# Optimization experiments

Hardware: AMD Instinct MI355X
Metric: run time of the kernel (lower is better)

Reference implementation:

```python
import jax, jax.numpy as jnp
from jax import lax
import numpy as np

N, L, C, G, K = 8, 4096, 256, 8, 3
GC = C // G
DILATION = 1
OFFSET_SCALE = 1.0
LN_EPS = 1e-6


def setup_inputs() -> dict:
    key = jax.random.key(0)
    ks = jax.random.split(key, 14)
    s = lambda k, shp, sc: jax.random.normal(k, shp, jnp.float32) * sc
    return {
        "x": jax.random.normal(ks[0], (N, L, C), jnp.float32),
        "W_in": s(ks[1], (C, C), (1.0 / C) ** 0.5),      # input_proj (in,out)
        "b_in": jnp.zeros((C,), jnp.float32),
        "conv_w": s(ks[2], (C, 1, K), 0.2),              # depthwise conv (O, I/g, K)
        "conv_b": jnp.zeros((C,), jnp.float32),
        "ln_g": jnp.ones((C,), jnp.float32),
        "ln_b": jnp.zeros((C,), jnp.float32),
        "W_off": s(ks[3], (C, G * K), 0.02),             # offset_linear
        "b_off": s(ks[4], (G * K,), 0.02),
        "W_mask": s(ks[5], (C, G * K), 0.02),            # mask_linear
        "b_mask": s(ks[6], (G * K,), 0.02),
        "W_out": s(ks[7], (C, C), (1.0 / C) ** 0.5),     # output_proj
        "b_out": jnp.zeros((C,), jnp.float32),
    }


def _dcnv3_1d(x, W_in, b_in, conv_w, conv_b, ln_g, ln_b,
              W_off, b_off, W_mask, b_mask, W_out, b_out):
    # x: (N, L, C)
    x_proj = x @ W_in + b_in                                     # (N,L,C)

    # depthwise conv -> LayerNorm(C) -> GELU  (the offset/mask feature branch)
    xc = x.transpose(0, 2, 1)                                    # (N,C,L)
    pad = (K - 1) // 2
    y = lax.conv_general_dilated(
        xc, conv_w, window_strides=(1,), padding=[(pad, pad)],
        dimension_numbers=("NCH", "OIH", "NCH"), feature_group_count=C)
    y = y + conv_b[None, :, None]
    y = y.transpose(0, 2, 1)                                     # (N,L,C)
    mu = y.mean(-1, keepdims=True)
    var = ((y - mu) ** 2).mean(-1, keepdims=True)
    y = (y - mu) * lax.rsqrt(var + LN_EPS) * ln_g + ln_b
    x_feat = jax.nn.gelu(y, approximate=False)                   # torch GELU = exact erf

    offset = (x_feat @ W_off + b_off).reshape(N, L, G, K)
    mask = jax.nn.softmax((x_feat @ W_mask + b_mask).reshape(N, L, G, K), axis=-1)

    # sampling locations (grid_sample with align_corners=True unnormalizes back to loc)
    ref_p = jnp.arange(L, dtype=jnp.float32)                     # (L,)
    lo = float(-((K - 1) // 2))
    hi = float((K - 1) // 2)
    dil_grid = jnp.linspace(lo, hi, K) * DILATION                # (K,)
    loc = ref_p[None, :, None, None] + dil_grid[None, None, None, :] \
          + offset * OFFSET_SCALE                                # (N,L,G,K)
    loc = jnp.remainder(loc, L)                                  # in [0, L)

    # bilinear sample along L with zero padding (matches F.grid_sample, H=1)
    f0 = jnp.floor(loc)
    w1 = loc - f0
    w0 = 1.0 - w1
    i0 = jnp.clip(f0.astype(jnp.int32), 0, L - 1)
    i1 = i0 + 1
    valid1 = (i1 < L)
    i1c = jnp.where(valid1, i1, 0)

    x_g = x_proj.reshape(N, L, G, GC)                            # (N,L,G,gc)
    nidx = jnp.arange(N)[:, None, None, None]
    gidx = jnp.arange(G)[None, None, :, None]
    v0 = x_g[nidx, i0, gidx]                                     # (N,L,G,K,gc)
    v1 = x_g[nidx, i1c, gidx] * valid1[..., None].astype(x_g.dtype)
    sampled = w0[..., None] * v0 + w1[..., None] * v1            # (N,L,G,K,gc)

    out = (sampled * mask[..., None]).sum(axis=3)                # (N,L,G,gc)
    out = out.reshape(N, L, C)
    return out @ W_out + b_out


def reference(x, W_in, b_in, conv_w, conv_b, ln_g, ln_b,
              W_off, b_off, W_mask, b_mask, W_out, b_out):
    return _dcnv3_1d(x, W_in, b_in, conv_w, conv_b, ln_g, ln_b,
                     W_off, b_off, W_mask, b_mask, W_out, b_out)
```

## Files before the change

kernel.cpp:

```cpp
#include <hip/hip_runtime.h>
#include <math.h>

constexpr int LL = 4096;
constexpr int CC = 256;
constexpr int MM = 32768;

typedef unsigned int u32;
typedef unsigned short u16;
typedef __attribute__((ext_vector_type(8))) short bf16x8;
typedef __attribute__((ext_vector_type(4))) float f32x4;

__device__ __forceinline__ u16 f2b(float f) {
    u32 u = __float_as_uint(f);
    u32 r = (u + 0x7fffu + ((u >> 16) & 1u)) >> 16;
    return (u16)r;
}
__device__ __forceinline__ u32 pack2(float a, float b) {
    return (u32)f2b(a) | ((u32)f2b(b) << 16);
}

__device__ __forceinline__ void gl_lds16(const u16* g, u16* l) {
    __builtin_amdgcn_global_load_lds(
        (const __attribute__((address_space(1))) unsigned int*)g,
        (__attribute__((address_space(3))) unsigned int*)l, 16, 0, 0);
}

__global__ __launch_bounds__(256) void conv_prep(
    const float* __restrict__ x, const float* __restrict__ cw,
    const float* __restrict__ cbias, const float* __restrict__ lng,
    const float* __restrict__ lnb, u16* __restrict__ xf,
    const float* __restrict__ W_in, const float* __restrict__ W_out,
    const float* __restrict__ W_off, const float* __restrict__ W_mask,
    u16* __restrict__ Wt_in, u16* __restrict__ Wt_out, u16* __restrict__ Wcomb)
{
    const int bid = blockIdx.x;
    const int t = threadIdx.x;
    if (bid >= 8192) {
        const int b = bid - 8192;
        if (b < 256) {
            Wt_in[b * 256 + t]  = f2b(W_in[t * 256 + b]);
            Wt_out[b * 256 + t] = f2b(W_out[t * 256 + b]);
        } else {
            const int j = b - 256;
            const float v = (j < 24) ? W_off[t * 24 + j] : W_mask[t * 24 + (j - 24)];
            Wcomb[j * 256 + t] = f2b(v);
        }
        return;
    }

    const int i = ((bid & 7) << 10) | (bid >> 3);

    const int wave = t >> 6;
    const int lane = t & 63;
    const int nl = (i << 2) + wave;
    const int l = nl & (LL - 1);
    const int c0 = lane << 2;
    const size_t base = (size_t)nl * CC + c0;

    float4 xc = *(const float4*)&x[base];
    float4 xm = make_float4(0.f, 0.f, 0.f, 0.f);
    float4 xp = make_float4(0.f, 0.f, 0.f, 0.f);
    if (l > 0)      xm = *(const float4*)&x[base - CC];
    if (l < LL - 1) xp = *(const float4*)&x[base + CC];

    float xmv[4] = {xm.x, xm.y, xm.z, xm.w};
    float xcv[4] = {xc.x, xc.y, xc.z, xc.w};
    float xpv[4] = {xp.x, xp.y, xp.z, xp.w};

    float y[4];
    float sum = 0.f, sq = 0.f;
#pragma unroll
    for (int j = 0; j < 4; ++j) {
        const int c = c0 + j;
        float v = fmaf(xmv[j], cw[c * 3 + 0],
                  fmaf(xcv[j], cw[c * 3 + 1],
                  fmaf(xpv[j], cw[c * 3 + 2], cbias[c])));
        y[j] = v;
        sum += v;
        sq  += v * v;
    }
#pragma unroll
    for (int off = 32; off > 0; off >>= 1) {
        sum += __shfl_xor(sum, off);
        sq  += __shfl_xor(sq, off);
    }
    const float mu  = sum * (1.f / CC);
    const float var = sq * (1.f / CC) - mu * mu;
    const float rs  = rsqrtf(var + 1e-6f);

    ushort4 o;
    float ov[4];
#pragma unroll
    for (int j = 0; j < 4; ++j) {
        const int c = c0 + j;
        const float tn = (y[j] - mu) * rs * lng[c] + lnb[c];
        ov[j] = 0.5f * tn * (1.f + erff(tn * 0.70710678118654752f));
    }
    o.x = f2b(ov[0]); o.y = f2b(ov[1]); o.z = f2b(ov[2]); o.w = f2b(ov[3]);
    *(ushort4*)&xf[base] = o;
}

__global__ __launch_bounds__(256, 2) void gemm1(
    const float* __restrict__ x, const u16* __restrict__ Wt_in,
    const float* __restrict__ b_in, u16* __restrict__ xprojb)
{
    __shared__ u16 As[2][128 * 32];
    __shared__ u16 Bs[2][128 * 32];

    const int t = threadIdx.x;
    const int w = t >> 6, lane = t & 63;
    const int lr = lane & 15, lk = lane >> 4;
    const int wm = w >> 1, wn = w & 1;

    const int d = blockIdx.x;
    const int m_t = (d & 7) * 32 + (d >> 4);
    const int n_t = (d >> 3) & 1;
    const int m0 = m_t * 128, n0 = n_t * 128;

    const int srow = lane >> 2;
    const int scol = (lane & 3) * 8;
    const int arow = t >> 1;
    const int akh = (t & 1) * 16;

    f32x4 acc[4][4];
#pragma unroll
    for (int i = 0; i < 4; ++i)
#pragma unroll
        for (int j = 0; j < 4; ++j) acc[i][j] = f32x4{0.f, 0.f, 0.f, 0.f};

    auto STAGE_B = [&](int buf, int kt) {
        const int k0 = kt * 32;
#pragma unroll
        for (int j = 0; j < 2; ++j) {
            const int rr = (w * 2 + j) * 16 + srow;
            gl_lds16(Wt_in + ((size_t)(n0 + rr) << 8) + k0 + scol,
                     &Bs[buf][0] + (w * 2 + j) * 512);
        }
    };
    const float* Abase = x + (size_t)(m0 + arow) * 256 + akh;

    {
        float4 f0 = *(const float4*)(Abase);
        float4 f1 = *(const float4*)(Abase + 4);
        float4 f2 = *(const float4*)(Abase + 8);
        float4 f3 = *(const float4*)(Abase + 12);
        STAGE_B(0, 0);
        u16* dst = &As[0][arow * 32 + akh];
        ((u32*)dst)[0] = pack2(f0.x, f0.y); ((u32*)dst)[1] = pack2(f0.z, f0.w);
        ((u32*)dst)[2] = pack2(f1.x, f1.y); ((u32*)dst)[3] = pack2(f1.z, f1.w);
        ((u32*)dst)[4] = pack2(f2.x, f2.y); ((u32*)dst)[5] = pack2(f2.z, f2.w);
        ((u32*)dst)[6] = pack2(f3.x, f3.y); ((u32*)dst)[7] = pack2(f3.z, f3.w);
    }

#pragma unroll
    for (int kt = 0; kt < 8; ++kt) {
        const int cur = kt & 1;
        __syncthreads();
        float4 f0, f1, f2, f3;
        if (kt < 7) {
            const float* ap = Abase + (kt + 1) * 32;
            f0 = *(const float4*)(ap);
            f1 = *(const float4*)(ap + 4);
            f2 = *(const float4*)(ap + 8);
            f3 = *(const float4*)(ap + 12);
            STAGE_B(cur ^ 1, kt + 1);
        }
        bf16x8 af[4], bfr[4];
#pragma unroll
        for (int mt = 0; mt < 4; ++mt)
            af[mt] = *(const bf16x8*)&As[cur][(wm * 64 + mt * 16 + lr) * 32 + lk * 8];
#pragma unroll
        for (int nt = 0; nt < 4; ++nt)
            bfr[nt] = *(const bf16x8*)&Bs[cur][(wn * 64 + nt * 16 + lr) * 32 + lk * 8];
#pragma unroll
        for (int mt = 0; mt < 4; ++mt)
#pragma unroll
            for (int nt = 0; nt < 4; ++nt)
                acc[mt][nt] = __builtin_amdgcn_mfma_f32_16x16x32_bf16(
                    af[mt], bfr[nt], acc[mt][nt], 0, 0, 0);
        if (kt < 7) {
            u16* dst = &As[cur ^ 1][arow * 32 + akh];
            ((u32*)dst)[0] = pack2(f0.x, f0.y); ((u32*)dst)[1] = pack2(f0.z, f0.w);
            ((u32*)dst)[2] = pack2(f1.x, f1.y); ((u32*)dst)[3] = pack2(f1.z, f1.w);
            ((u32*)dst)[4] = pack2(f2.x, f2.y); ((u32*)dst)[5] = pack2(f2.z, f2.w);
            ((u32*)dst)[6] = pack2(f3.x, f3.y); ((u32*)dst)[7] = pack2(f3.z, f3.w);
        }
    }

    const int r0 = lk * 4;
#pragma unroll
    for (int nt = 0; nt < 4; ++nt) {
        const int cn = n0 + wn * 64 + nt * 16 + lr;
        const float bv = b_in[cn];
#pragma unroll
        for (int mt = 0; mt < 4; ++mt)
#pragma unroll
            for (int r4 = 0; r4 < 4; ++r4)
                xprojb[(size_t)(m0 + wm * 64 + mt * 16 + r0 + r4) * 256 + cn] =
                    f2b(acc[mt][nt][r4] + bv);
    }
}

__global__ __launch_bounds__(256, 2) void offmask_gemm(
    const u16* __restrict__ xfeatb, const u16* __restrict__ xprojb,
    const u16* __restrict__ Wcomb, const float* __restrict__ boff,
    const float* __restrict__ bmask, const u16* __restrict__ Wt_out,
    const float* __restrict__ b_out, float* __restrict__ out)
{
    __shared__ __align__(16) char s_mem[32768];
    __shared__ uint2 s_pack[512 * 3];
    float* logit = (float*)s_mem;

    const int t = threadIdx.x;
    const int w = t >> 6, lane = t & 63;
    const int lr = lane & 15, lk8 = (lane >> 4) * 8;
    const int r0 = (lane >> 4) * 4;
    const int d = blockIdx.x;
    const int blk = ((d & 7) << 6) | (d >> 3);
    const size_t row0 = (size_t)blk * 64;

    f32x4 pacc[3];
#pragma unroll
    for (int ct = 0; ct < 3; ++ct) pacc[ct] = f32x4{0.f, 0.f, 0.f, 0.f};
    const u16* fbase = xfeatb + (row0 + w * 16 + lr) * 256;
#pragma unroll
    for (int ks = 0; ks < 8; ++ks) {
        const int ke = ks * 32 + lk8;
        bf16x8 a = *(const bf16x8*)(fbase + ke);
#pragma unroll
        for (int ct = 0; ct < 3; ++ct) {
            bf16x8 bfr = *(const bf16x8*)(Wcomb + (size_t)(ct * 16 + lr) * 256 + ke);
            pacc[ct] = __builtin_amdgcn_mfma_f32_16x16x32_bf16(a, bfr, pacc[ct], 0, 0, 0);
        }
    }
#pragma unroll
    for (int ct = 0; ct < 3; ++ct) {
        const int j = ct * 16 + lr;
        const float bj = (j < 24) ? boff[j] : bmask[j - 24];
#pragma unroll
        for (int r4 = 0; r4 < 4; ++r4)
            logit[(w * 16 + r0 + r4) * 50 + j] = pacc[ct][r4] + bj;
    }
    __syncthreads();

#pragma unroll
    for (int pi = 0; pi < 2; ++pi) {
        const int pp = pi * 256 + t;
        const int rw = pp >> 3, g = pp & 7;
        const float* lp = &logit[rw * 50];
        const float m0v = lp[24 + g * 3 + 0];
        const float m1v = lp[24 + g * 3 + 1];
        const float m2v = lp[24 + g * 3 + 2];
        const float mx = fmaxf(m0v, fmaxf(m1v, m2v));
        const float e0 = expf(m0v - mx), e1 = expf(m1v - mx), e2 = expf(m2v - mx);
        const float inv = 1.f / (e0 + e1 + e2);
        const float msk[3] = {e0 * inv, e1 * inv, e2 * inv};
        const float lf = (float)((blk & 63) * 64 + rw);
#pragma unroll
        for (int k = 0; k < 3; ++k) {
            const float loc = lf + (float)(k - 1) + lp[g * 3 + k];
            float r = fmodf(loc, (float)LL);
            if (r < 0.f) r += (float)LL;
            const float f0 = floorf(r);
            int i0 = (int)f0;
            i0 = i0 < 0 ? 0 : (i0 > LL - 1 ? LL - 1 : i0);
            const int i1 = i0 + 1;
            const float w1 = r - f0;
            const bool valid = (i1 < LL);
            union { u32 uw; _Float16 h[2]; } uh;
            uh.h[0] = (_Float16)(msk[k] * (1.f - w1));
            uh.h[1] = (_Float16)(valid ? msk[k] * w1 : 0.f);
            const u32 ij = (u32)i0 | ((u32)(valid ? i1 : 0) << 16);
            s_pack[pp * 3 + k] = make_uint2(uh.uw, ij);
        }
    }
    __syncthreads();

    {
        const int ig = t >> 5, tc = t & 31;
        const int c0 = tc * 8, g4 = tc >> 2;
        const u16* xpn = xprojb + (size_t)(blk >> 6) * LL * 256;
        const int ibeg = ig * 8;
#pragma unroll 4
        for (int i = ibeg; i < ibeg + 8; ++i) {
            const int bidx = (i * 8 + g4) * 3;
            float v[8] = {0.f, 0.f, 0.f, 0.f, 0.f, 0.f, 0.f, 0.f};
#pragma unroll
            for (int k = 0; k < 3; ++k) {
                const uint2 pk = s_pack[bidx + k];
                union { u32 uw; _Float16 h[2]; } uh; uh.uw = pk.x;
                const float wa = (float)uh.h[0], wb = (float)uh.h[1];
                const int i0 = (int)(pk.y & 0xffffu), i1 = (int)(pk.y >> 16);
                uint4 ua = *(const uint4*)(xpn + (size_t)i0 * 256 + c0);
                uint4 ub = *(const uint4*)(xpn + (size_t)i1 * 256 + c0);
                const u32 au[4] = {ua.x, ua.y, ua.z, ua.w};
                const u32 bu[4] = {ub.x, ub.y, ub.z, ub.w};
#pragma unroll
                for (int j = 0; j < 4; ++j) {
                    v[2 * j]     = fmaf(wa, __uint_as_float(au[j] << 16),
                                   fmaf(wb, __uint_as_float(bu[j] << 16), v[2 * j]));
                    v[2 * j + 1] = fmaf(wa, __uint_as_float(au[j] & 0xffff0000u),
                                   fmaf(wb, __uint_as_float(bu[j] & 0xffff0000u), v[2 * j + 1]));
                }
            }
            uint4 wd;
            wd.x = pack2(v[0], v[1]); wd.y = pack2(v[2], v[3]);
            wd.z = pack2(v[4], v[5]); wd.w = pack2(v[6], v[7]);
            const int addr = (i * 512 + tc * 16) ^ ((i & 7) << 4);
            *(uint4*)(s_mem + addr) = wd;
        }
    }
    __syncthreads();

    f32x4 acc[4][4];
#pragma unroll
    for (int i = 0; i < 4; ++i)
#pragma unroll
        for (int j = 0; j < 4; ++j) acc[i][j] = f32x4{0.f, 0.f, 0.f, 0.f};

    const u16* Bw = Wt_out + (size_t)(w * 64) * 256;
#pragma unroll
    for (int ks = 0; ks < 8; ++ks) {
        bf16x8 af[4], bfr[4];
#pragma unroll
        for (int mt = 0; mt < 4; ++mt) {
            const int rm = mt * 16 + lr;
            const int addr = (rm * 512 + ks * 64 + lk8 * 2) ^ ((rm & 7) << 4);
            af[mt] = *(const bf16x8*)(s_mem + addr);
        }
        const int ke = ks * 32 + lk8;
#pragma unroll
        for (int nt = 0; nt < 4; ++nt)
            bfr[nt] = *(const bf16x8*)(Bw + (size_t)(nt * 16 + lr) * 256 + ke);
#pragma unroll
        for (int mt = 0; mt < 4; ++mt)
#pragma unroll
            for (int nt = 0; nt < 4; ++nt)
                acc[mt][nt] = __builtin_amdgcn_mfma_f32_16x16x32_bf16(
                    af[mt], bfr[nt], acc[mt][nt], 0, 0, 0);
    }
#pragma unroll
    for (int nt = 0; nt < 4; ++nt) {
        const int cn = w * 64 + nt * 16 + lr;
        const float bv = b_out[cn];
#pragma unroll
        for (int mt = 0; mt < 4; ++mt)
#pragma unroll
            for (int r4 = 0; r4 < 4; ++r4)
                out[(row0 + mt * 16 + r0 + r4) * 256 + cn] = acc[mt][nt][r4] + bv;
    }
}

extern "C" void kernel_launch(void* const* d_in, const int* in_sizes, int n_in,
                              void* d_out, int out_size, void* d_ws, size_t ws_size,
                              hipStream_t stream)
{
    const float* x      = (const float*)d_in[0];
    const float* W_in   = (const float*)d_in[1];
    const float* b_in   = (const float*)d_in[2];
    const float* conv_w = (const float*)d_in[3];
    const float* conv_b = (const float*)d_in[4];
    const float* ln_g   = (const float*)d_in[5];
    const float* ln_b   = (const float*)d_in[6];
    const float* W_off  = (const float*)d_in[7];
    const float* b_off  = (const float*)d_in[8];
    const float* W_mask = (const float*)d_in[9];
    const float* b_mask = (const float*)d_in[10];
    const float* W_out  = (const float*)d_in[11];
    const float* b_out  = (const float*)d_in[12];

    u16* xfeatb = (u16*)d_ws;
    u16* xprojb = (u16*)((char*)d_ws + 16777216);
    char* wsb   = (char*)d_ws + 33554432;
    u16* Wt_in  = (u16*)(wsb);
    u16* Wt_out = (u16*)(wsb + 131072);
    u16* Wcombp = (u16*)(wsb + 262144);

    conv_prep<<<8192 + 304, 256, 0, stream>>>(x, conv_w, conv_b, ln_g, ln_b, xfeatb,
                                              W_in, W_out, W_off, W_mask,
                                              Wt_in, Wt_out, Wcombp);
    gemm1<<<512, 256, 0, stream>>>(x, Wt_in, b_in, xprojb);
    offmask_gemm<<<512, 256, 0, stream>>>(xfeatb, xprojb, Wcombp, b_off, b_mask,
                                          Wt_out, b_out, (float*)d_out);
}
```

Before: 70.11 us.

## Stage local x_proj window in LDS for deformable sampling gathers

Preloads a 68-row halo window of x_proj (plus wraparound rows for edge blocks) into shared memory with async global-to-LDS loads, overlapped with the offset/mask GEMM. The sampling pass then reads neighbors from LDS via per-sample slot indices and falls back to global memory only when an offset lands outside the window. This removes repeated scattered global gathers, at the cost of 36KB of extra LDS per block, which may lower occupancy, and extra branching in the gather loop.

```diff
diff --git a/kernel.cpp b/kernel.cpp
--- a/kernel.cpp
+++ b/kernel.cpp
@@ -207,6 +207,7 @@
     const float* __restrict__ bmask, const u16* __restrict__ Wt_out,
     const float* __restrict__ b_out, float* __restrict__ out)
 {
+    __shared__ __align__(16) u16 win[72 * 256];
     __shared__ __align__(16) char s_mem[32768];
     __shared__ uint2 s_pack[512 * 3];
     float* logit = (float*)s_mem;
@@ -218,6 +219,28 @@
     const int d = blockIdx.x;
     const int blk = ((d & 7) << 6) | (d >> 3);
     const size_t row0 = (size_t)blk * 64;
+    const int seq = blk >> 6;
+    const int l0s = (blk & 63) * 64;
+
+    {
+        const u16* xps = xprojb + (((size_t)seq) << 12) * 256;
+#pragma unroll
+        for (int pass = 0; pass < 9; ++pass) {
+            const int chunk = pass * 256 + t;
+            const int slot = chunk >> 5;
+            const int cc = (chunk & 31) << 4;
+            int lsrc; bool valid;
+            if (slot < 68) { lsrc = l0s - 2 + slot; valid = (lsrc >= 0) && (lsrc < LL); }
+            else if (l0s == 0)       { lsrc = 4092 + (slot - 68); valid = true; }
+            else if (l0s == LL - 64) { lsrc = slot - 68;          valid = true; }
+            else { lsrc = 0; valid = false; }
+            u16* ldst = win + (size_t)(pass * 256 + w * 64) * 8;
+            if (valid) {
+                const int sb = cc ^ ((slot & 7) << 4);
+                gl_lds16(xps + (size_t)lsrc * 256 + (sb >> 1), ldst);
+            }
+        }
+    }
 
     f32x4 pacc[3];
 #pragma unroll
@@ -255,7 +278,7 @@
         const float e0 = expf(m0v - mx), e1 = expf(m1v - mx), e2 = expf(m2v - mx);
         const float inv = 1.f / (e0 + e1 + e2);
         const float msk[3] = {e0 * inv, e1 * inv, e2 * inv};
-        const float lf = (float)((blk & 63) * 64 + rw);
+        const float lf = (float)(l0s + rw);
 #pragma unroll
         for (int k = 0; k < 3; ++k) {
             const float loc = lf + (float)(k - 1) + lp[g * 3 + k];
@@ -267,11 +290,21 @@
             const int i1 = i0 + 1;
             const float w1 = r - f0;
             const bool valid = (i1 < LL);
+            const float wa = msk[k] * (1.f - w1);
+            const float wb = valid ? msk[k] * w1 : 0.f;
+            auto slotOf = [&](int iv) -> u32 {
+                const int dsx = iv - l0s + 2;
+                if ((u32)dsx < 68u) return (u32)dsx;
+                if (l0s == 0 && iv >= 4092)      return (u32)(68 + iv - 4092);
+                if (l0s == LL - 64 && iv < 4)    return (u32)(68 + iv);
+                return 0xffu;
+            };
+            const u32 s0 = slotOf(i0);
+            const u32 s1 = valid ? slotOf(i1) : s0;
             union { u32 uw; _Float16 h[2]; } uh;
-            uh.h[0] = (_Float16)(msk[k] * (1.f - w1));
-            uh.h[1] = (_Float16)(valid ? msk[k] * w1 : 0.f);
-            const u32 ij = (u32)i0 | ((u32)(valid ? i1 : 0) << 16);
-            s_pack[pp * 3 + k] = make_uint2(uh.uw, ij);
+            uh.h[0] = (_Float16)wa;
+            uh.h[1] = (_Float16)wb;
+            s_pack[pp * 3 + k] = make_uint2(uh.uw, s0 | (s1 << 8) | ((u32)i0 << 16));
         }
     }
     __syncthreads();
@@ -279,9 +312,9 @@
     {
         const int ig = t >> 5, tc = t & 31;
         const int c0 = tc * 8, g4 = tc >> 2;
-        const u16* xpn = xprojb + (size_t)(blk >> 6) * LL * 256;
+        const u16* xpn = xprojb + (((size_t)seq) << 12) * 256;
         const int ibeg = ig * 8;
-#pragma unroll 4
+#pragma unroll 2
         for (int i = ibeg; i < ibeg + 8; ++i) {
             const int bidx = (i * 8 + g4) * 3;
             float v[8] = {0.f, 0.f, 0.f, 0.f, 0.f, 0.f, 0.f, 0.f};
@@ -290,9 +323,19 @@
                 const uint2 pk = s_pack[bidx + k];
                 union { u32 uw; _Float16 h[2]; } uh; uh.uw = pk.x;
                 const float wa = (float)uh.h[0], wb = (float)uh.h[1];
-                const int i0 = (int)(pk.y & 0xffffu), i1 = (int)(pk.y >> 16);
-                uint4 ua = *(const uint4*)(xpn + (size_t)i0 * 256 + c0);
-                uint4 ub = *(const uint4*)(xpn + (size_t)i1 * 256 + c0);
+                const u32 s0 = pk.y & 0xffu, s1 = (pk.y >> 8) & 0xffu;
+                const int i0g = (int)(pk.y >> 16);
+                uint4 ua, ub;
+                if (s0 != 0xffu)
+                    ua = *(const uint4*)((const char*)win +
+                         (((int)s0 * 512 + tc * 16) ^ (((int)s0 & 7) << 4)));
+                else
+                    ua = *(const uint4*)(xpn + (size_t)i0g * 256 + c0);
+                if (s1 != 0xffu)
+                    ub = *(const uint4*)((const char*)win +
+                         (((int)s1 * 512 + tc * 16) ^ (((int)s1 & 7) << 4)));
+                else
+                    ub = *(const uint4*)(xpn + (size_t)(i0g + 1) * 256 + c0);
                 const u32 au[4] = {ua.x, ua.y, ua.z, ua.w};
                 const u32 bu[4] = {ub.x, ub.y, ub.z, ub.w};
 #pragma unroll
```

Measured after the change: 72.95 us. +4.1%, slower.
